# Optimization experiments

Hardware: AMD Instinct MI355X
Metric: run time of the kernel (lower is better)

The kernel has to match this reference:

```python
import jax, jax.numpy as jnp
import numpy as np

# ---- fixed dims (match init_kwargs / input_specs) ----
B = 8           # number of graphs in the batch
N_PER = 2048    # points per graph
N = B * N_PER   # total source nodes
F = 128         # in_channels
RATIO = 32      # seed nodes per graph
H, C = 4, 32    # GATv2 heads, per-head out channels (H*C == 128)
T = B * RATIO   # total target (seed) nodes
E = N * RATIO   # dense bipartite edges
NEG_SLOPE = 0.2


def setup_inputs() -> dict:
    key = jax.random.key(0)
    ks = jax.random.split(key, 6)
    x = jax.random.normal(ks[0], (N, F), jnp.float32)
    # regular batch assignment: nodes sorted by graph id
    batch = jnp.repeat(jnp.arange(B, dtype=jnp.int32), N_PER)
    seed_nodes = jax.random.normal(ks[1], (RATIO, F), jnp.float32)
    # GATv2Conv params (glorot-ish scale)
    W_l = jax.random.normal(ks[2], (F, H * C), jnp.float32) / np.sqrt(F)
    W_r = jax.random.normal(ks[3], (F, H * C), jnp.float32) / np.sqrt(F)
    att = jax.random.normal(ks[4], (H, C), jnp.float32) / np.sqrt(C)
    bias = jax.random.normal(ks[5], (H * C,), jnp.float32) * 0.01
    return {"x": x, "batch": batch, "seed_nodes": seed_nodes,
            "W_l": W_l, "W_r": W_r, "att": att, "bias": bias}


def reference(x, batch, seed_nodes, W_l, W_r, att, bias):
    batch = batch.astype(jnp.int32)
    # seed nodes replicated per graph: x_aggrs = seed_nodes.repeat(B, 1)
    x_dst = jnp.tile(seed_nodes, (B, 1))                    # [T, F]
    # dense bipartite edge list (as in the torch module)
    src = jnp.repeat(jnp.arange(N, dtype=jnp.int32), RATIO)         # [E]
    tgt = jnp.tile(jnp.arange(RATIO, dtype=jnp.int32), N) \
          + jnp.repeat(batch, RATIO) * RATIO                        # [E]
    # GATv2Conv bipartite message passing
    h_src = (x @ W_l).reshape(N, H, C)                      # [N, H, C]
    h_dst = (x_dst @ W_r).reshape(T, H, C)                  # [T, H, C]
    h_j = h_src[src]                                        # [E, H, C] gather
    h_i = h_dst[tgt]                                        # [E, H, C] gather
    e = jax.nn.leaky_relu(h_i + h_j, NEG_SLOPE)             # [E, H, C]
    logit = jnp.einsum('ehc,hc->eh', e, att)                # [E, H]
    # segment softmax over edges grouped by target node
    m = jax.ops.segment_max(logit, tgt, num_segments=T)     # [T, H]
    p = jnp.exp(logit - m[tgt])                             # [E, H]
    s = jax.ops.segment_sum(p, tgt, num_segments=T)         # [T, H]
    alpha = p / s[tgt]                                      # [E, H]
    # weighted aggregation (scatter-add)
    out = jax.ops.segment_sum(alpha[:, :, None] * h_j, tgt, num_segments=T)
    out = out.reshape(T, H * C) + bias                      # [T, 128]
    new_batch = jnp.repeat(jnp.arange(B, dtype=jnp.int32), RATIO)   # [T]
    return out, new_batch
```

## Files before the change

kernel.cpp:

```cpp
#include <hip/hip_runtime.h>
#include <hip/hip_bf16.h>

#define N_NODES 16384
#define F_DIM   128
#define B_GR    8
#define N_PERG  2048
#define RATIO   32
#define T_TGT   256
#define HC      128
#define NEG     0.2f

typedef unsigned short u16;
typedef unsigned int   u32;
typedef short bf16x8 __attribute__((ext_vector_type(8)));
typedef float f32x4  __attribute__((ext_vector_type(4)));

__device__ __forceinline__ float bf2f(u16 u){ union{u32 i; float f;} v; v.i=((u32)u)<<16; return v.f; }
__device__ __forceinline__ u16 f2bf(float f){ __hip_bfloat16 b = __float2bfloat16(f); return *(u16*)&b; }

#define HS_OFF    0u
#define WLT_OFF   16384u
#define SPART_OFF 49152u
#define PART_OFF  180224u

__global__ void __launch_bounds__(256) k0_prep(
    const float* __restrict__ seed, const float* __restrict__ Wr,
    const float* __restrict__ Wl, float* __restrict__ hs, u16* __restrict__ WlT){
  int bid = blockIdx.x, t = threadIdx.x;
  if (bid < 32){
    int r = bid, c = t & 127, kh = t >> 7;
    const float* sr = seed + r*F_DIM + kh*64;
    const float* wr = Wr + (size_t)kh*64*HC + c;
    float a = 0.f;
    #pragma unroll 8
    for (int f=0; f<64; ++f) a = fmaf(sr[f], wr[(size_t)f*HC], a);
    __shared__ float red[256];
    red[t] = a; __syncthreads();
    if (kh == 0) hs[r*HC + c] = red[c] + red[128 + c];
  } else {
    int gid = (bid-32)*256 + t;
    int c = gid >> 7, k = gid & 127;
    WlT[c*F_DIM + k] = f2bf(Wl[(size_t)k*HC + c]);
  }
}

__global__ void __launch_bounds__(256) k1_fused(
    const float* __restrict__ x, const u16* __restrict__ WlT,
    const float* __restrict__ att, const float* __restrict__ hs,
    float* __restrict__ partial, float* __restrict__ spart){
  __shared__ u16 hssh[32*40];
  __shared__ u16 hT[32*72];
  __shared__ u16 hN[64*40];
  __shared__ u16 eT[32*72];
  int t = threadIdx.x;
  int chunk = blockIdx.x & 255, h = blockIdx.x >> 8;
  int j0 = chunk * 64;
  int lane = t & 63, w = t >> 6;
  int arow = lane & 15, kgrp = lane >> 4;

  #pragma unroll
  for (int i=0;i<4;++i){
    int idx = i*256 + t;
    int r = idx >> 3, c4 = (idx & 7) * 4;
    float4 v = *(const float4*)&hs[r*HC + h*32 + c4];
    union{ u16 s[4]; uint2 u; } pk;
    pk.s[0]=f2bf(v.x); pk.s[1]=f2bf(v.y); pk.s[2]=f2bf(v.z); pk.s[3]=f2bf(v.w);
    *(uint2*)&hssh[r*40 + c4] = pk.u;
  }

  const float* xrow = x + (size_t)(j0 + w*16 + arow)*F_DIM + kgrp*8;
  const u16* wb0 = WlT + (size_t)(h*32 +      arow)*F_DIM + kgrp*8;
  const u16* wb1 = WlT + (size_t)(h*32 + 16 + arow)*F_DIM + kgrp*8;
  f32x4 acc0 = {0.f,0.f,0.f,0.f}, acc1 = {0.f,0.f,0.f,0.f};
  #pragma unroll
  for (int ks=0; ks<4; ++ks){
    float4 alo = *(const float4*)(xrow + ks*32);
    float4 ahi = *(const float4*)(xrow + ks*32 + 4);
    union { u16 s[8]; bf16x8 v; } af;
    af.s[0]=f2bf(alo.x); af.s[1]=f2bf(alo.y); af.s[2]=f2bf(alo.z); af.s[3]=f2bf(alo.w);
    af.s[4]=f2bf(ahi.x); af.s[5]=f2bf(ahi.y); af.s[6]=f2bf(ahi.z); af.s[7]=f2bf(ahi.w);
    bf16x8 b0 = *(const bf16x8*)(wb0 + ks*32);
    bf16x8 b1 = *(const bf16x8*)(wb1 + ks*32);
    acc0 = __builtin_amdgcn_mfma_f32_16x16x32_bf16(af.v, b0, acc0, 0, 0, 0);
    acc1 = __builtin_amdgcn_mfma_f32_16x16x32_bf16(af.v, b1, acc1, 0, 0, 0);
  }
  {
    int nbase = w*16 + kgrp*4;
    union { u16 s[4]; uint2 v; } p0, p1;
    #pragma unroll
    for (int reg=0; reg<4; ++reg){ p0.s[reg] = f2bf(acc0[reg]); p1.s[reg] = f2bf(acc1[reg]); }
    *(uint2*)&hT[(arow     )*72 + nbase] = p0.v;
    *(uint2*)&hT[(16 + arow)*72 + nbase] = p1.v;
    #pragma unroll
    for (int reg=0; reg<4; ++reg){
      hN[(nbase+reg)*40 + arow]      = p0.s[reg];
      hN[(nbase+reg)*40 + 16 + arow] = p1.s[reg];
    }
  }
  __syncthreads();

  {
    int n = lane;
    float hv[32];
    #pragma unroll
    for (int m=0;m<4;++m){
      uint4 q = *(const uint4*)&hN[n*40 + m*8];
      const u16* qs = (const u16*)&q;
      #pragma unroll
      for (int e=0;e<8;++e) hv[m*8+e] = bf2f(qs[e]);
    }
    float attv[32];
    #pragma unroll
    for (int m=0;m<8;++m){
      float4 a4 = *(const float4*)&att[h*32 + m*4];
      attv[m*4+0]=a4.x; attv[m*4+1]=a4.y; attv[m*4+2]=a4.z; attv[m*4+3]=a4.w;
    }
    #pragma unroll
    for (int ri=0; ri<8; ++ri){
      int r = w*8 + ri;
      float p = 0.f;
      #pragma unroll
      for (int m=0;m<4;++m){
        uint4 q = *(const uint4*)&hssh[r*40 + m*8];
        const u16* qs = (const u16*)&q;
        #pragma unroll
        for (int e=0;e<8;++e){
          float v = bf2f(qs[e]) + hv[m*8+e];
          v = fmaxf(v, NEG*v);
          p = fmaf(attv[m*8+e], v, p);
        }
      }
      eT[r*72 + n] = f2bf(__expf(p));
    }
  }
  __syncthreads();

  if (t < 32){
    float s = 0.f;
    #pragma unroll
    for (int m=0;m<8;++m){
      uint4 q = *(const uint4*)&eT[t*72 + m*8];
      const u16* qs = (const u16*)&q;
      #pragma unroll
      for (int e=0;e<8;++e) s += bf2f(qs[e]);
    }
    int b = chunk >> 5, c32 = chunk & 31;
    spart[(size_t)(b*32 + c32)*128 + h*32 + t] = s;
  }

  {
    int mt = w >> 1, ct = w & 1;
    const u16* ea = eT + (mt*16 + arow)*72 + kgrp*8;
    const u16* hb = hT + (ct*16 + arow)*72 + kgrp*8;
    f32x4 oacc = {0.f,0.f,0.f,0.f};
    #pragma unroll
    for (int ks=0; ks<2; ++ks){
      bf16x8 av = *(const bf16x8*)(ea + ks*32);
      bf16x8 bv = *(const bf16x8*)(hb + ks*32);
      oacc = __builtin_amdgcn_mfma_f32_16x16x32_bf16(av, bv, oacc, 0, 0, 0);
    }
    int b = chunk >> 5, c32 = chunk & 31;
    size_t obase = ((size_t)c32*T_TGT + (size_t)b*RATIO + mt*16 + kgrp*4)*HC
                 + h*32 + ct*16 + arow;
    #pragma unroll
    for (int reg=0; reg<4; ++reg)
      partial[obase + (size_t)reg*HC] = oacc[reg];
  }
}

__global__ void __launch_bounds__(256) k4_final(
    const float* __restrict__ partial, const float* __restrict__ spart,
    const float* __restrict__ bias, float* __restrict__ out){
  int bid = blockIdx.x, t = threadIdx.x;
  if (bid == 128){
    out[T_TGT*HC + t] = (float)(t >> 5);
    return;
  }
  __shared__ float ssh[8];
  int g = t >> 5, lane = t & 31;
  int trow = bid*2 + (g>>2);
  int b = trow >> 5, r = trow & 31, h = g & 3;
  float s = spart[(size_t)(b*32 + lane)*128 + h*32 + r];
  s += __shfl_xor(s,1,32); s += __shfl_xor(s,2,32);
  s += __shfl_xor(s,4,32); s += __shfl_xor(s,8,32); s += __shfl_xor(s,16,32);
  if (lane == 0) ssh[g] = 1.0f / s;
  __syncthreads();
  int id = bid*256 + t;
  int k = id & 127, h2 = k >> 5, lr = t >> 7;
  float v = 0.f;
  #pragma unroll
  for (int ch=0; ch<32; ++ch) v += partial[(size_t)ch*T_TGT*HC + id];
  out[id] = v * ssh[lr*4 + h2] + bias[k];
}

extern "C" void kernel_launch(void* const* d_in, const int* in_sizes, int n_in,
                              void* d_out, int out_size, void* d_ws, size_t ws_size,
                              hipStream_t stream){
  const float* x    = (const float*)d_in[0];
  const float* seed = (const float*)d_in[2];
  const float* Wl   = (const float*)d_in[3];
  const float* Wr   = (const float*)d_in[4];
  const float* att  = (const float*)d_in[5];
  const float* bias = (const float*)d_in[6];

  char* ws = (char*)d_ws;
  float* hs    = (float*)(ws + HS_OFF);
  u16*   WlT   = (u16*)  (ws + WLT_OFF);
  float* spart = (float*)(ws + SPART_OFF);
  float* part  = (float*)(ws + PART_OFF);

  k0_prep <<<96,   256, 0, stream>>>(seed, Wr, Wl, hs, WlT);
  k1_fused<<<1024, 256, 0, stream>>>(x, WlT, att, hs, part, spart);
  k4_final<<<129,  256, 0, stream>>>(part, spart, bias, (float*)d_out);
}
```

Baseline: 27.69 us.

## Rewrite leaky-ReLU logit via abs identity and double block threads

The GATv2 logit is rewritten with leaky_relu(v)=0.6v+0.4|v|. The linear part splits into a per-source term plus a per-target term (att·h_dst), precomputed in the prep kernel. The fused kernel now launches 512 threads per block, so each wave computes one 16x16 MFMA tile and scores 4 target rows instead of 8. The bf16 shared-memory copy of h_dst is dropped; h_dst is read directly from global memory as fp32. Half the waves sit idle during the aggregation MFMA, and the softmax denominator sum moves to a spare wave so it runs alongside the MFMAs.

```diff
diff --git a/kernel.cpp b/kernel.cpp
--- a/kernel.cpp
+++ b/kernel.cpp
@@ -8,7 +8,6 @@
 #define RATIO   32
 #define T_TGT   256
 #define HC      128
-#define NEG     0.2f
 
 typedef unsigned short u16;
 typedef unsigned int   u32;
@@ -19,13 +18,15 @@
 __device__ __forceinline__ u16 f2bf(float f){ __hip_bfloat16 b = __float2bfloat16(f); return *(u16*)&b; }
 
 #define HS_OFF    0u
-#define WLT_OFF   16384u
-#define SPART_OFF 49152u
-#define PART_OFF  180224u
+#define D_OFF     16384u
+#define WLT_OFF   16896u
+#define SPART_OFF 49664u
+#define PART_OFF  180736u
 
 __global__ void __launch_bounds__(256) k0_prep(
     const float* __restrict__ seed, const float* __restrict__ Wr,
-    const float* __restrict__ Wl, float* __restrict__ hs, u16* __restrict__ WlT){
+    const float* __restrict__ Wl, const float* __restrict__ att,
+    float* __restrict__ hs, float* __restrict__ dlin, u16* __restrict__ WlT){
   int bid = blockIdx.x, t = threadIdx.x;
   if (bid < 32){
     int r = bid, c = t & 127, kh = t >> 7;
@@ -37,6 +38,15 @@
     __shared__ float red[256];
     red[t] = a; __syncthreads();
     if (kh == 0) hs[r*HC + c] = red[c] + red[128 + c];
+    if (t < 4){
+      float dd = 0.f;
+      #pragma unroll
+      for (int cc=0; cc<32; ++cc){
+        int ci = t*32 + cc;
+        dd = fmaf(att[ci], red[ci] + red[128 + ci], dd);
+      }
+      dlin[r*4 + t] = dd;
+    }
   } else {
     int gid = (bid-32)*256 + t;
     int c = gid >> 7, k = gid & 127;
@@ -44,11 +54,11 @@
   }
 }
 
-__global__ void __launch_bounds__(256) k1_fused(
+__global__ void __launch_bounds__(512, 8) k1_fused(
     const float* __restrict__ x, const u16* __restrict__ WlT,
     const float* __restrict__ att, const float* __restrict__ hs,
+    const float* __restrict__ dlin,
     float* __restrict__ partial, float* __restrict__ spart){
-  __shared__ u16 hssh[32*40];
   __shared__ u16 hT[32*72];
   __shared__ u16 hN[64*40];
   __shared__ u16 eT[32*72];
@@ -57,21 +67,11 @@
   int j0 = chunk * 64;
   int lane = t & 63, w = t >> 6;
   int arow = lane & 15, kgrp = lane >> 4;
-
-  #pragma unroll
-  for (int i=0;i<4;++i){
-    int idx = i*256 + t;
-    int r = idx >> 3, c4 = (idx & 7) * 4;
-    float4 v = *(const float4*)&hs[r*HC + h*32 + c4];
-    union{ u16 s[4]; uint2 u; } pk;
-    pk.s[0]=f2bf(v.x); pk.s[1]=f2bf(v.y); pk.s[2]=f2bf(v.z); pk.s[3]=f2bf(v.w);
-    *(uint2*)&hssh[r*40 + c4] = pk.u;
-  }
-
-  const float* xrow = x + (size_t)(j0 + w*16 + arow)*F_DIM + kgrp*8;
-  const u16* wb0 = WlT + (size_t)(h*32 +      arow)*F_DIM + kgrp*8;
-  const u16* wb1 = WlT + (size_t)(h*32 + 16 + arow)*F_DIM + kgrp*8;
-  f32x4 acc0 = {0.f,0.f,0.f,0.f}, acc1 = {0.f,0.f,0.f,0.f};
+  int n0 = (w >> 1) * 16, c0 = (w & 1) * 16;
+
+  const float* xrow = x + (size_t)(j0 + n0 + arow)*F_DIM + kgrp*8;
+  const u16* wb = WlT + (size_t)(h*32 + c0 + arow)*F_DIM + kgrp*8;
+  f32x4 acc = {0.f,0.f,0.f,0.f};
   #pragma unroll
   for (int ks=0; ks<4; ++ks){
     float4 alo = *(const float4*)(xrow + ks*32);
@@ -79,76 +79,58 @@
     union { u16 s[8]; bf16x8 v; } af;
     af.s[0]=f2bf(alo.x); af.s[1]=f2bf(alo.y); af.s[2]=f2bf(alo.z); af.s[3]=f2bf(alo.w);
     af.s[4]=f2bf(ahi.x); af.s[5]=f2bf(ahi.y); af.s[6]=f2bf(ahi.z); af.s[7]=f2bf(ahi.w);
-    bf16x8 b0 = *(const bf16x8*)(wb0 + ks*32);
-    bf16x8 b1 = *(const bf16x8*)(wb1 + ks*32);
-    acc0 = __builtin_amdgcn_mfma_f32_16x16x32_bf16(af.v, b0, acc0, 0, 0, 0);
-    acc1 = __builtin_amdgcn_mfma_f32_16x16x32_bf16(af.v, b1, acc1, 0, 0, 0);
+    bf16x8 bv = *(const bf16x8*)(wb + ks*32);
+    acc = __builtin_amdgcn_mfma_f32_16x16x32_bf16(af.v, bv, acc, 0, 0, 0);
   }
   {
-    int nbase = w*16 + kgrp*4;
-    union { u16 s[4]; uint2 v; } p0, p1;
-    #pragma unroll
-    for (int reg=0; reg<4; ++reg){ p0.s[reg] = f2bf(acc0[reg]); p1.s[reg] = f2bf(acc1[reg]); }
-    *(uint2*)&hT[(arow     )*72 + nbase] = p0.v;
-    *(uint2*)&hT[(16 + arow)*72 + nbase] = p1.v;
-    #pragma unroll
-    for (int reg=0; reg<4; ++reg){
-      hN[(nbase+reg)*40 + arow]      = p0.s[reg];
-      hN[(nbase+reg)*40 + 16 + arow] = p1.s[reg];
-    }
+    union { u16 s[4]; uint2 v; } pk;
+    #pragma unroll
+    for (int reg=0; reg<4; ++reg) pk.s[reg] = f2bf(acc[reg]);
+    *(uint2*)&hT[(c0+arow)*72 + n0 + kgrp*4] = pk.v;
+    #pragma unroll
+    for (int reg=0; reg<4; ++reg)
+      hN[(n0 + kgrp*4 + reg)*40 + c0 + arow] = pk.s[reg];
   }
   __syncthreads();
 
   {
-    int n = lane;
-    float hv[32];
-    #pragma unroll
-    for (int m=0;m<4;++m){
-      uint4 q = *(const uint4*)&hN[n*40 + m*8];
+    int n = lane, r0 = w*4;
+    float pabs0=0.f, pabs1=0.f, pabs2=0.f, pabs3=0.f, g=0.f;
+    #pragma unroll
+    for (int cc=0; cc<4; ++cc){
+      uint4 q = *(const uint4*)&hN[n*40 + cc*8];
       const u16* qs = (const u16*)&q;
-      #pragma unroll
-      for (int e=0;e<8;++e) hv[m*8+e] = bf2f(qs[e]);
-    }
-    float attv[32];
-    #pragma unroll
-    for (int m=0;m<8;++m){
-      float4 a4 = *(const float4*)&att[h*32 + m*4];
-      attv[m*4+0]=a4.x; attv[m*4+1]=a4.y; attv[m*4+2]=a4.z; attv[m*4+3]=a4.w;
-    }
-    #pragma unroll
-    for (int ri=0; ri<8; ++ri){
-      int r = w*8 + ri;
-      float p = 0.f;
-      #pragma unroll
-      for (int m=0;m<4;++m){
-        uint4 q = *(const uint4*)&hssh[r*40 + m*8];
-        const u16* qs = (const u16*)&q;
-        #pragma unroll
-        for (int e=0;e<8;++e){
-          float v = bf2f(qs[e]) + hv[m*8+e];
-          v = fmaxf(v, NEG*v);
-          p = fmaf(attv[m*8+e], v, p);
-        }
+      float hv[8];
+      #pragma unroll
+      for (int e=0;e<8;++e) hv[e] = bf2f(qs[e]);
+      const float* ap  = att + h*32 + cc*8;
+      const float* h0p = hs + (size_t)(r0  )*HC + h*32 + cc*8;
+      const float* h1p = hs + (size_t)(r0+1)*HC + h*32 + cc*8;
+      const float* h2p = hs + (size_t)(r0+2)*HC + h*32 + cc*8;
+      const float* h3p = hs + (size_t)(r0+3)*HC + h*32 + cc*8;
+      #pragma unroll
+      for (int e=0;e<8;++e){
+        float a = ap[e], hvv = hv[e];
+        g     = fmaf(a, hvv, g);
+        pabs0 = fmaf(a, __builtin_fabsf(hvv + h0p[e]), pabs0);
+        pabs1 = fmaf(a, __builtin_fabsf(hvv + h1p[e]), pabs1);
+        pabs2 = fmaf(a, __builtin_fabsf(hvv + h2p[e]), pabs2);
+        pabs3 = fmaf(a, __builtin_fabsf(hvv + h3p[e]), pabs3);
       }
-      eT[r*72 + n] = f2bf(__expf(p));
-    }
+    }
+    float p0 = fmaf(0.4f, pabs0, 0.6f*(g + dlin[(r0  )*4 + h]));
+    float p1 = fmaf(0.4f, pabs1, 0.6f*(g + dlin[(r0+1)*4 + h]));
+    float p2 = fmaf(0.4f, pabs2, 0.6f*(g + dlin[(r0+2)*4 + h]));
+    float p3 = fmaf(0.4f, pabs3, 0.6f*(g + dlin[(r0+3)*4 + h]));
+    eT[(r0  )*72 + n] = f2bf(__expf(p0));
+    eT[(r0+1)*72 + n] = f2bf(__expf(p1));
+    eT[(r0+2)*72 + n] = f2bf(__expf(p2));
+    eT[(r0+3)*72 + n] = f2bf(__expf(p3));
   }
   __syncthreads();
 
-  if (t < 32){
-    float s = 0.f;
-    #pragma unroll
-    for (int m=0;m<8;++m){
-      uint4 q = *(const uint4*)&eT[t*72 + m*8];
-      const u16* qs = (const u16*)&q;
-      #pragma unroll
-      for (int e=0;e<8;++e) s += bf2f(qs[e]);
-    }
-    int b = chunk >> 5, c32 = chunk & 31;
-    spart[(size_t)(b*32 + c32)*128 + h*32 + t] = s;
-  }
-
-  {
+  int b = chunk >> 5, c32 = chunk & 31;
+  if (w < 4){
     int mt = w >> 1, ct = w & 1;
     const u16* ea = eT + (mt*16 + arow)*72 + kgrp*8;
     const u16* hb = hT + (ct*16 + arow)*72 + kgrp*8;
@@ -159,12 +141,22 @@
       bf16x8 bv = *(const bf16x8*)(hb + ks*32);
       oacc = __builtin_amdgcn_mfma_f32_16x16x32_bf16(av, bv, oacc, 0, 0, 0);
     }
-    int b = chunk >> 5, c32 = chunk & 31;
     size_t obase = ((size_t)c32*T_TGT + (size_t)b*RATIO + mt*16 + kgrp*4)*HC
                  + h*32 + ct*16 + arow;
     #pragma unroll
     for (int reg=0; reg<4; ++reg)
       partial[obase + (size_t)reg*HC] = oacc[reg];
+  } else if (w == 4 && lane < 32){
+    int r = lane;
+    float s = 0.f;
+    #pragma unroll
+    for (int m=0;m<8;++m){
+      uint4 q = *(const uint4*)&eT[r*72 + m*8];
+      const u16* qs = (const u16*)&q;
+      #pragma unroll
+      for (int e=0;e<8;++e) s += bf2f(qs[e]);
+    }
+    spart[(size_t)(b*32 + c32)*128 + h*32 + r] = s;
   }
 }
 
@@ -205,11 +197,12 @@
 
   char* ws = (char*)d_ws;
   float* hs    = (float*)(ws + HS_OFF);
+  float* dlin  = (float*)(ws + D_OFF);
   u16*   WlT   = (u16*)  (ws + WLT_OFF);
   float* spart = (float*)(ws + SPART_OFF);
   float* part  = (float*)(ws + PART_OFF);
 
-  k0_prep <<<96,   256, 0, stream>>>(seed, Wr, Wl, hs, WlT);
-  k1_fused<<<1024, 256, 0, stream>>>(x, WlT, att, hs, part, spart);
+  k0_prep <<<96,   256, 0, stream>>>(seed, Wr, Wl, att, hs, dlin, WlT);
+  k1_fused<<<1024, 512, 0, stream>>>(x, WlT, att, hs, dlin, part, spart);
   k4_final<<<129,  256, 0, stream>>>(part, spart, bias, (float*)d_out);
 }
```

Result: slower. 35.15 us (+27.0%).

## Rewrite leaky-ReLU logit as linear plus abs term with precomputed dot products

Applied to the files above, without the earlier changes.

Uses leaky_relu(v)=0.6v+0.4|v| so the linear part of the attention logit splits into a per-source dot (att·h_j) and a per-target dot (att·h_i). The per-target part is precomputed in the prep kernel, which removes the max and multiply from the inner loop. The LDS staging of hs and the node features moves from bf16 to fp32, dropping the conversions at the cost of more shared memory. A launch-bounds occupancy hint is added to the fused kernel.

```diff
diff --git a/kernel.cpp b/kernel.cpp
--- a/kernel.cpp
+++ b/kernel.cpp
@@ -8,7 +8,6 @@
 #define RATIO   32
 #define T_TGT   256
 #define HC      128
-#define NEG     0.2f
 
 typedef unsigned short u16;
 typedef unsigned int   u32;
@@ -19,13 +18,15 @@
 __device__ __forceinline__ u16 f2bf(float f){ __hip_bfloat16 b = __float2bfloat16(f); return *(u16*)&b; }
 
 #define HS_OFF    0u
-#define WLT_OFF   16384u
-#define SPART_OFF 49152u
-#define PART_OFF  180224u
+#define D_OFF     16384u
+#define WLT_OFF   16896u
+#define SPART_OFF 49664u
+#define PART_OFF  180736u
 
 __global__ void __launch_bounds__(256) k0_prep(
     const float* __restrict__ seed, const float* __restrict__ Wr,
-    const float* __restrict__ Wl, float* __restrict__ hs, u16* __restrict__ WlT){
+    const float* __restrict__ Wl, const float* __restrict__ att,
+    float* __restrict__ hs, float* __restrict__ dlin, u16* __restrict__ WlT){
   int bid = blockIdx.x, t = threadIdx.x;
   if (bid < 32){
     int r = bid, c = t & 127, kh = t >> 7;
@@ -37,6 +38,15 @@
     __shared__ float red[256];
     red[t] = a; __syncthreads();
     if (kh == 0) hs[r*HC + c] = red[c] + red[128 + c];
+    if (t < 4){
+      float dd = 0.f;
+      #pragma unroll
+      for (int cc=0; cc<32; ++cc){
+        int ci = t*32 + cc;
+        dd = fmaf(att[ci], red[ci] + red[128 + ci], dd);
+      }
+      dlin[r*4 + t] = dd;
+    }
   } else {
     int gid = (bid-32)*256 + t;
     int c = gid >> 7, k = gid & 127;
@@ -44,28 +54,24 @@
   }
 }
 
-__global__ void __launch_bounds__(256) k1_fused(
+__global__ void __launch_bounds__(256, 4) k1_fused(
     const float* __restrict__ x, const u16* __restrict__ WlT,
     const float* __restrict__ att, const float* __restrict__ hs,
+    const float* __restrict__ dlin,
     float* __restrict__ partial, float* __restrict__ spart){
-  __shared__ u16 hssh[32*40];
-  __shared__ u16 hT[32*72];
-  __shared__ u16 hN[64*40];
-  __shared__ u16 eT[32*72];
+  __shared__ u16   hT[32*72];
+  __shared__ float hN[64*36];
+  __shared__ float hssh[32*36];
+  __shared__ u16   eT[32*72];
   int t = threadIdx.x;
   int chunk = blockIdx.x & 255, h = blockIdx.x >> 8;
   int j0 = chunk * 64;
   int lane = t & 63, w = t >> 6;
   int arow = lane & 15, kgrp = lane >> 4;
 
-  #pragma unroll
-  for (int i=0;i<4;++i){
-    int idx = i*256 + t;
-    int r = idx >> 3, c4 = (idx & 7) * 4;
-    float4 v = *(const float4*)&hs[r*HC + h*32 + c4];
-    union{ u16 s[4]; uint2 u; } pk;
-    pk.s[0]=f2bf(v.x); pk.s[1]=f2bf(v.y); pk.s[2]=f2bf(v.z); pk.s[3]=f2bf(v.w);
-    *(uint2*)&hssh[r*40 + c4] = pk.u;
+  {
+    int r = t >> 3, cq = (t & 7) * 4;
+    *(float4*)&hssh[r*36 + cq] = *(const float4*)&hs[r*HC + h*32 + cq];
   }
 
   const float* xrow = x + (size_t)(j0 + w*16 + arow)*F_DIM + kgrp*8;
@@ -93,48 +99,44 @@
     *(uint2*)&hT[(16 + arow)*72 + nbase] = p1.v;
     #pragma unroll
     for (int reg=0; reg<4; ++reg){
-      hN[(nbase+reg)*40 + arow]      = p0.s[reg];
-      hN[(nbase+reg)*40 + 16 + arow] = p1.s[reg];
+      hN[(nbase+reg)*36 + arow]      = acc0[reg];
+      hN[(nbase+reg)*36 + 16 + arow] = acc1[reg];
     }
   }
   __syncthreads();
 
   {
-    int n = lane;
-    float hv[32];
-    #pragma unroll
-    for (int m=0;m<4;++m){
-      uint4 q = *(const uint4*)&hN[n*40 + m*8];
-      const u16* qs = (const u16*)&q;
-      #pragma unroll
-      for (int e=0;e<8;++e) hv[m*8+e] = bf2f(qs[e]);
-    }
-    float attv[32];
+    int n = lane, r0 = w*8;
+    float hv[32], attv[32];
     #pragma unroll
     for (int m=0;m<8;++m){
+      float4 q = *(const float4*)&hN[n*36 + m*4];
+      hv[m*4+0]=q.x; hv[m*4+1]=q.y; hv[m*4+2]=q.z; hv[m*4+3]=q.w;
       float4 a4 = *(const float4*)&att[h*32 + m*4];
       attv[m*4+0]=a4.x; attv[m*4+1]=a4.y; attv[m*4+2]=a4.z; attv[m*4+3]=a4.w;
     }
+    float g = 0.f;
+    #pragma unroll
+    for (int c=0;c<32;++c) g = fmaf(attv[c], hv[c], g);
     #pragma unroll
     for (int ri=0; ri<8; ++ri){
-      int r = w*8 + ri;
-      float p = 0.f;
+      int r = r0 + ri;
+      float pabs = 0.f;
       #pragma unroll
-      for (int m=0;m<4;++m){
-        uint4 q = *(const uint4*)&hssh[r*40 + m*8];
-        const u16* qs = (const u16*)&q;
-        #pragma unroll
-        for (int e=0;e<8;++e){
-          float v = bf2f(qs[e]) + hv[m*8+e];
-          v = fmaxf(v, NEG*v);
-          p = fmaf(attv[m*8+e], v, p);
-        }
+      for (int m=0;m<8;++m){
+        float4 hsq = *(const float4*)&hssh[r*36 + m*4];
+        pabs = fmaf(attv[m*4+0], __builtin_fabsf(hsq.x + hv[m*4+0]), pabs);
+        pabs = fmaf(attv[m*4+1], __builtin_fabsf(hsq.y + hv[m*4+1]), pabs);
+        pabs = fmaf(attv[m*4+2], __builtin_fabsf(hsq.z + hv[m*4+2]), pabs);
+        pabs = fmaf(attv[m*4+3], __builtin_fabsf(hsq.w + hv[m*4+3]), pabs);
       }
+      float p = fmaf(0.4f, pabs, 0.6f*(g + dlin[r*4 + h]));
       eT[r*72 + n] = f2bf(__expf(p));
     }
   }
   __syncthreads();
 
+  int b = chunk >> 5, c32 = chunk & 31;
   if (t < 32){
     float s = 0.f;
     #pragma unroll
@@ -144,10 +146,8 @@
       #pragma unroll
       for (int e=0;e<8;++e) s += bf2f(qs[e]);
     }
-    int b = chunk >> 5, c32 = chunk & 31;
     spart[(size_t)(b*32 + c32)*128 + h*32 + t] = s;
   }
-
   {
     int mt = w >> 1, ct = w & 1;
     const u16* ea = eT + (mt*16 + arow)*72 + kgrp*8;
@@ -159,7 +159,6 @@
       bf16x8 bv = *(const bf16x8*)(hb + ks*32);
       oacc = __builtin_amdgcn_mfma_f32_16x16x32_bf16(av, bv, oacc, 0, 0, 0);
     }
-    int b = chunk >> 5, c32 = chunk & 31;
     size_t obase = ((size_t)c32*T_TGT + (size_t)b*RATIO + mt*16 + kgrp*4)*HC
                  + h*32 + ct*16 + arow;
     #pragma unroll
@@ -205,11 +204,12 @@
 
   char* ws = (char*)d_ws;
   float* hs    = (float*)(ws + HS_OFF);
+  float* dlin  = (float*)(ws + D_OFF);
   u16*   WlT   = (u16*)  (ws + WLT_OFF);
   float* spart = (float*)(ws + SPART_OFF);
   float* part  = (float*)(ws + PART_OFF);
 
-  k0_prep <<<96,   256, 0, stream>>>(seed, Wr, Wl, hs, WlT);
-  k1_fused<<<1024, 256, 0, stream>>>(x, WlT, att, hs, part, spart);
+  k0_prep <<<96,   256, 0, stream>>>(seed, Wr, Wl, att, hs, dlin, WlT);
+  k1_fused<<<1024, 256, 0, stream>>>(x, WlT, att, hs, dlin, part, spart);
   k4_final<<<129,  256, 0, stream>>>(part, spart, bias, (float*)d_out);
 }
```

Result: faster. 25.41 us (-8.2%).
